# Performance work log

Measured on AMD Instinct MI355X. Metric: run time of the kernel, lower is better.

Reference implementation:

```python
import jax, jax.numpy as jnp
import numpy as np

EPS_LN = 1e-5

def _ln(x, g, b):
    m = x.mean(-1, keepdims=True)
    v = jnp.var(x, axis=-1, keepdims=True)
    return (x - m) * jax.lax.rsqrt(v + EPS_LN) * g + b


def _forward(x, edge_attr, lin0_w, lin0_b, enn_w1, enn_b1, enn_g1, enn_b1n,
             enn_w2, enn_b2, enn_g2, enn_b2n, conv_bias,
             gru_w_ih, gru_w_hh, gru_b_ih, gru_b_hh,
             lstm_w_ih, lstm_w_hh, lstm_b_ih, lstm_b_hh,
             lin1_w, lin1_b, lin1_g, lin1_bn, lin2_w, lin2_b,
             edge_index, target_index, target_class):
    N = x.shape[0]
    D = lin0_w.shape[0]
    src, dst = edge_index[0], edge_index[1]

    out = jax.nn.relu(x @ lin0_w.T + lin0_b)            # [N, D]
    h = out                                             # GRU hidden state

    # edge NN -> per-edge weight matrix [E, D, D] (edge_attr constant across iters)
    e1 = jax.nn.relu(_ln(edge_attr @ enn_w1.T + enn_b1, enn_g1, enn_b1n))
    ew = _ln(e1 @ enn_w2.T + enn_b2, enn_g2, enn_b2n).reshape(-1, D, D)

    counts = jnp.clip(jax.ops.segment_sum(jnp.ones_like(dst, jnp.float32), dst, num_segments=N), 1.0)[:, None]

    for _ in range(3):
        msg = jnp.einsum('ed,edo->eo', out[src], ew)     # per-edge matmul
        agg = jax.ops.segment_sum(msg, dst, num_segments=N) / counts  # scatter-mean
        m = jax.nn.relu(agg + conv_bias)
        # GRU cell (seq len 1)
        gx = m @ gru_w_ih.T + gru_b_ih
        gh = h @ gru_w_hh.T + gru_b_hh
        xr, xz, xn = jnp.split(gx, 3, axis=-1)
        hr, hz, hn = jnp.split(gh, 3, axis=-1)
        r = jax.nn.sigmoid(xr + hr)
        z = jax.nn.sigmoid(xz + hz)
        n = jnp.tanh(xn + r * hn)
        h = (1.0 - z) * n + z * h
        out = h

    # Set2Set with batch_index = arange(N) (each node is its own set), 3 steps
    idx = jnp.arange(N)
    hl = jnp.zeros((N, D), x.dtype)
    cl = jnp.zeros((N, D), x.dtype)
    q_star = jnp.zeros((N, 2 * D), x.dtype)
    for _ in range(3):
        g = q_star @ lstm_w_ih.T + lstm_b_ih + hl @ lstm_w_hh.T + lstm_b_hh
        gi, gf, gg, go = jnp.split(g, 4, axis=-1)
        cl = jax.nn.sigmoid(gf) * cl + jax.nn.sigmoid(gi) * jnp.tanh(gg)
        hl = jax.nn.sigmoid(go) * jnp.tanh(cl)
        q = hl
        e = (out * q[idx]).sum(-1, keepdims=True)
        emax = jax.ops.segment_max(e, idx, num_segments=N)
        a = jnp.exp(e - emax[idx])
        a = a / (jax.ops.segment_sum(a, idx, num_segments=N)[idx] + 1e-16)
        r_pool = jax.ops.segment_sum(a * out, idx, num_segments=N)
        q_star = jnp.concatenate([q, r_pool], axis=-1)

    a0, a1 = target_index[0], target_index[1]
    cat = jnp.concatenate([out[a0], out[a1], q_star[a0], q_star[a1]], axis=-1)  # [P, 6D]
    p = jax.nn.relu(_ln(cat @ lin1_w.T + lin1_b, lin1_g, lin1_bn))
    p = p @ lin2_w.T + lin2_b                           # [P, 8]
    return jnp.take_along_axis(p, target_class[:, None], axis=1)[:, 0]


def setup_inputs() -> dict:
    N, E, P, F, D = 10000, 20000, 15000, 16, 64
    ks = iter(jax.random.split(jax.random.key(0), 40))
    def nrm(shape, s=0.1):
        return jax.random.normal(next(ks), shape, jnp.float32) * s
    return {
        'x': jax.random.normal(next(ks), (N, F), jnp.float32),
        'edge_attr': jax.random.normal(next(ks), (E, 4), jnp.float32),
        'lin0_w': nrm((D, F)), 'lin0_b': jnp.zeros((D,), jnp.float32),
        'enn_w1': nrm((128, 4)), 'enn_b1': jnp.zeros((128,), jnp.float32),
        'enn_g1': jnp.ones((128,), jnp.float32), 'enn_b1n': jnp.zeros((128,), jnp.float32),
        'enn_w2': nrm((D * D, 128), 0.05), 'enn_b2': jnp.zeros((D * D,), jnp.float32),
        'enn_g2': jnp.ones((D * D,), jnp.float32), 'enn_b2n': jnp.zeros((D * D,), jnp.float32),
        'conv_bias': jnp.zeros((D,), jnp.float32),
        'gru_w_ih': nrm((3 * D, D)), 'gru_w_hh': nrm((3 * D, D)),
        'gru_b_ih': jnp.zeros((3 * D,), jnp.float32), 'gru_b_hh': jnp.zeros((3 * D,), jnp.float32),
        'lstm_w_ih': nrm((4 * D, 2 * D)), 'lstm_w_hh': nrm((4 * D, D)),
        'lstm_b_ih': jnp.zeros((4 * D,), jnp.float32), 'lstm_b_hh': jnp.zeros((4 * D,), jnp.float32),
        'lin1_w': nrm((D, 6 * D)), 'lin1_b': jnp.zeros((D,), jnp.float32),
        'lin1_g': jnp.ones((D,), jnp.float32), 'lin1_bn': jnp.zeros((D,), jnp.float32),
        'lin2_w': nrm((8, D)), 'lin2_b': jnp.zeros((8,), jnp.float32),
        'edge_index': jax.random.randint(next(ks), (2, E), 0, N),
        'target_index': jax.random.randint(next(ks), (2, P), 0, N),
        'target_class': jax.random.randint(next(ks), (P,), 0, 8),
    }


def reference(x, edge_attr, lin0_w, lin0_b, enn_w1, enn_b1, enn_g1, enn_b1n,
              enn_w2, enn_b2, enn_g2, enn_b2n, conv_bias,
              gru_w_ih, gru_w_hh, gru_b_ih, gru_b_hh,
              lstm_w_ih, lstm_w_hh, lstm_b_ih, lstm_b_hh,
              lin1_w, lin1_b, lin1_g, lin1_bn, lin2_w, lin2_b,
              edge_index, target_index, target_class):
    return _forward(x, edge_attr, lin0_w, lin0_b, enn_w1, enn_b1, enn_g1, enn_b1n,
                    enn_w2, enn_b2, enn_g2, enn_b2n, conv_bias,
                    gru_w_ih, gru_w_hh, gru_b_ih, gru_b_hh,
                    lstm_w_ih, lstm_w_hh, lstm_b_ih, lstm_b_hh,
                    lin1_w, lin1_b, lin1_g, lin1_bn, lin2_w, lin2_b,
                    edge_index, target_index, target_class)
```

## Files before the change

### kernel.cpp

```cpp
#include <hip/hip_runtime.h>
#include <hip/hip_bf16.h>

#define EPS_LN 1e-5f

typedef __attribute__((ext_vector_type(8))) short bf16x8;
typedef __attribute__((ext_vector_type(4))) float f32x4;

__device__ __forceinline__ float dot4(float4 a, float4 b) {
    return a.x * b.x + a.y * b.y + a.z * b.z + a.w * b.w;
}
__device__ __forceinline__ float sigmoidf_(float x) { return 1.0f / (1.0f + expf(-x)); }

__device__ __forceinline__ float bfu2f(unsigned short u) {
    unsigned v = ((unsigned)u) << 16;
    float f;
    __builtin_memcpy(&f, &v, 4);
    return f;
}
__device__ __forceinline__ unsigned short f2bfu(float f) {
    __hip_bfloat16 h = __float2bfloat16(f);
    unsigned short u;
    __builtin_memcpy(&u, &h, 2);
    return u;
}
__device__ __forceinline__ unsigned pack2bf(float a, float b) {
    return (unsigned)f2bfu(a) | ((unsigned)f2bfu(b) << 16);
}
__device__ __forceinline__ void async_cp16(void* lds, const void* g) {
    __builtin_amdgcn_global_load_lds((const __attribute__((address_space(1))) void*)g,
                                     (__attribute__((address_space(3))) void*)lds, 16, 0, 0);
}

__global__ void init_kernel(const float* __restrict__ x, const float* __restrict__ w,
                            const float* __restrict__ b, float* __restrict__ h,
                            const int* __restrict__ ei, float* __restrict__ counts,
                            int N, int E) {
    int id = blockIdx.x * blockDim.x + threadIdx.x;
    if (id < N * 64) {
        int n = id >> 6, o = id & 63;
        const float* xr = x + n * 16;
        const float* wr = w + o * 16;
        float acc = b[o];
#pragma unroll
        for (int k = 0; k < 16; k++) acc += xr[k] * wr[k];
        h[id] = fmaxf(acc, 0.0f);
    }
    if (id < E) atomicAdd(&counts[ei[E + id]], 1.0f);
}

__global__ __launch_bounds__(128) void edge_nn1_kernel(
    const float* __restrict__ ea, const float* __restrict__ w1, const float* __restrict__ b1,
    const float* __restrict__ g1, const float* __restrict__ b1n,
    unsigned short* __restrict__ e1h, unsigned short* __restrict__ e1l, int E) {
    int e = blockIdx.x, j = threadIdx.x;
    float a0 = ea[e * 4 + 0], a1 = ea[e * 4 + 1], a2 = ea[e * 4 + 2], a3 = ea[e * 4 + 3];
    const float* wr = w1 + j * 4;
    float z = b1[j] + a0 * wr[0] + a1 * wr[1] + a2 * wr[2] + a3 * wr[3];
    float s = z, s2 = z * z;
#pragma unroll
    for (int m = 32; m >= 1; m >>= 1) { s += __shfl_xor(s, m); s2 += __shfl_xor(s2, m); }
    __shared__ float ls[2], ls2[2];
    int wv = j >> 6;
    if ((j & 63) == 0) { ls[wv] = s; ls2[wv] = s2; }
    __syncthreads();
    float S = ls[0] + ls[1], S2 = ls2[0] + ls2[1];
    float mu = S * (1.0f / 128.0f);
    float var = fmaxf(S2 * (1.0f / 128.0f) - mu * mu, 0.0f);
    float inv = rsqrtf(var + EPS_LN);
    float v = fmaxf((z - mu) * inv * g1[j] + b1n[j], 0.0f);
    unsigned short hi = f2bfu(v);
    unsigned short lo = f2bfu(v - bfu2f(hi));
    int jp = j ^ ((e & 7) << 3);
    e1h[e * 128 + jp] = hi;
    e1l[e * 128 + jp] = lo;
}

__global__ __launch_bounds__(128) void mpart_kernel(const float* __restrict__ w2,
                                                    const float* __restrict__ b2,
                                                    const float* __restrict__ g2,
                                                    unsigned short* __restrict__ w2gp,
                                                    float* __restrict__ b2g,
                                                    float* __restrict__ pMT, float* __restrict__ pv,
                                                    float* __restrict__ pcw, float* __restrict__ psb,
                                                    float* __restrict__ pc) {
    __shared__ float wL[16][128];
    __shared__ float b2L[16];
    int t = threadIdx.x, b = blockIdx.x;
#pragma unroll
    for (int i = 0; i < 16; i++) {
        int idx = t + i * 128;
        wL[idx >> 7][idx & 127] = w2[(size_t)(b * 16 + (idx >> 7)) * 128 + (idx & 127)];
    }
    if (t < 16) b2L[t] = b2[b * 16 + t];
    __syncthreads();
#pragma unroll
    for (int o = 0; o < 16; o++) {
        int r = b * 16 + o;
        int x = (r & 63) >> 1;
        int jj = (r >> 6) + ((r & 1) << 6);
        w2gp[(size_t)x * 16384 + jj * 128 + (t ^ ((jj & 7) << 3))] = f2bfu(wL[o][t] * g2[r]);
    }
    if (t < 16) b2g[b * 16 + t] = b2L[t] * g2[b * 16 + t];
    int j = t;
    float wj[16];
#pragma unroll
    for (int o = 0; o < 16; o++) wj[o] = wL[o][j];
    float pvj = 0.f, pcwj = 0.f;
#pragma unroll
    for (int o = 0; o < 16; o++) { pvj += wj[o] * b2L[o]; pcwj += wj[o]; }
    for (int i4 = 0; i4 < 32; i4++) {
        float4 a = {0.f, 0.f, 0.f, 0.f};
#pragma unroll
        for (int o = 0; o < 16; o++) {
            float4 w4 = *(const float4*)&wL[o][i4 * 4];
            a.x += wj[o] * w4.x; a.y += wj[o] * w4.y;
            a.z += wj[o] * w4.z; a.w += wj[o] * w4.w;
        }
        *(float4*)&pMT[((size_t)b * 128 + j) * 128 + i4 * 4] = a;
    }
    pv[b * 128 + j] = pvj;
    pcw[b * 128 + j] = pcwj;
    if (t == 0) {
        float sb = 0.f, cc = 0.f;
#pragma unroll
        for (int o = 0; o < 16; o++) { sb += b2L[o]; cc += b2L[o] * b2L[o]; }
        psb[b] = sb;
        pc[b] = cc;
    }
}

__global__ __launch_bounds__(256) void mreduce_kernel(const float* __restrict__ pMT,
                                                      const float* __restrict__ pv,
                                                      const float* __restrict__ pcw,
                                                      const float* __restrict__ psb,
                                                      const float* __restrict__ pc,
                                                      unsigned short* __restrict__ mb,
                                                      float* __restrict__ varr,
                                                      float* __restrict__ cw,
                                                      float* __restrict__ sbc) {
    int fid = blockIdx.x * 256 + threadIdx.x;
    float s = 0.f;
    int j = fid >> 7, i = fid & 127;
    for (int b = 0; b < 256; b++) s += pMT[((size_t)b * 128 + j) * 128 + i];
    mb[fid] = f2bfu(s);
    if (fid < 128) {
        float sv = 0.f, sc = 0.f;
        for (int b = 0; b < 256; b++) { sv += pv[b * 128 + fid]; sc += pcw[b * 128 + fid]; }
        varr[fid] = sv;
        cw[fid] = sc;
    }
    if (fid == 0) {
        float sb = 0.f, cc = 0.f;
        for (int b = 0; b < 256; b++) { sb += psb[b]; cc += pc[b]; }
        sbc[0] = sb;
        sbc[1] = cc;
    }
}

__global__ __launch_bounds__(256) void stats_kernel(
    const unsigned short* __restrict__ e1h, const unsigned short* __restrict__ e1l,
    const unsigned short* __restrict__ mb, const float* __restrict__ cw,
    const float* __restrict__ varr, const float* __restrict__ sbc,
    float* __restrict__ stats, int E) {
    __shared__ __align__(16) unsigned char smem[65536];
    const int t = threadIdx.x;
    const int eb = blockIdx.x * 64;
#pragma unroll
    for (int r = 0; r < 4; r++) {
        int idx = t + r * 256;
        int row = idx >> 4, kseg = idx & 15;
        int er = eb + row;
        if (er >= E) er = E - 1;
        uint4 vh = *(const uint4*)&e1h[(size_t)er * 128 + kseg * 8];
        uint4 vl = *(const uint4*)&e1l[(size_t)er * 128 + kseg * 8];
        int off = row * 256 + kseg * 16;
        *(uint4*)(smem + off) = vh;
        *(uint4*)(smem + 16384 + off) = vl;
    }
#pragma unroll
    for (int r = 0; r < 8; r++) {
        int idx = t + r * 256;
        int row = idx >> 4, kseg = idx & 15;
        uint4 v = *(const uint4*)&mb[(size_t)row * 128 + kseg * 8];
        *(uint4*)(smem + 32768 + row * 256 + ((kseg * 16) ^ ((row & 7) << 4))) = v;
    }
    __syncthreads();
    const int w = t >> 6, lane = t & 63;
    const int wrow = w * 16;
    const int r16 = lane & 15, kg = lane >> 4;
    f32x4 tacc[8];
#pragma unroll
    for (int nj = 0; nj < 8; nj++) tacc[nj] = (f32x4){0.f, 0.f, 0.f, 0.f};
#pragma unroll
    for (int ks = 0; ks < 4; ks++) {
        int arow = wrow + r16;
        int koff = ks * 64 + kg * 16;
        bf16x8 ah = *(const bf16x8*)(smem + arow * 256 + (koff ^ ((arow & 7) << 4)));
        bf16x8 al = *(const bf16x8*)(smem + 16384 + arow * 256 + (koff ^ ((arow & 7) << 4)));
#pragma unroll
        for (int nj = 0; nj < 8; nj++) {
            int brow = nj * 16 + r16;
            bf16x8 bf = *(const bf16x8*)(smem + 32768 + brow * 256 + (koff ^ ((brow & 7) << 4)));
            tacc[nj] = __builtin_amdgcn_mfma_f32_16x16x32_bf16(ah, bf, tacc[nj], 0, 0, 0);
            tacc[nj] = __builtin_amdgcn_mfma_f32_16x16x32_bf16(al, bf, tacc[nj], 0, 0, 0);
        }
    }
    __syncthreads();
#pragma unroll
    for (int nj = 0; nj < 8; nj++)
#pragma unroll
        for (int r = 0; r < 4; r++) {
            int row = wrow + kg * 4 + r, col = nj * 16 + r16;
            *(float*)(smem + 32768 + row * 512 + col * 4) = tacc[nj][r];
        }
    __syncthreads();
    int el = t >> 2, q = t & 3;
    float s2p = 0.f, sp = 0.f, svp = 0.f;
    for (int kk = 0; kk < 32; kk++) {
        int k = q * 32 + kk;
        int boff = el * 256 + ((2 * k) ^ ((el & 7) << 4));
        float e1v = bfu2f(*(const unsigned short*)(smem + boff)) +
                    bfu2f(*(const unsigned short*)(smem + 16384 + boff));
        float tv = *(const float*)(smem + 32768 + el * 512 + k * 4);
        s2p += tv * e1v;
        sp += e1v * cw[k];
        svp += e1v * varr[k];
    }
    s2p += __shfl_xor(s2p, 1); s2p += __shfl_xor(s2p, 2);
    sp += __shfl_xor(sp, 1);   sp += __shfl_xor(sp, 2);
    svp += __shfl_xor(svp, 1); svp += __shfl_xor(svp, 2);
    if (q == 0) {
        int e = eb + el;
        if (e < E) {
            float S = sp + sbc[0];
            float S2 = s2p + 2.f * svp + sbc[1];
            float mu = S * (1.0f / 4096.0f);
            float var = fmaxf(S2 * (1.0f / 4096.0f) - mu * mu, 0.0f);
            float inv = rsqrtf(var + EPS_LN);
            stats[e * 2 + 0] = inv;
            stats[e * 2 + 1] = mu * inv;
        }
    }
}

__global__ __launch_bounds__(256) void zgemm_final(
    const unsigned short* __restrict__ e1h,
    const unsigned short* __restrict__ w2gp, const float* __restrict__ b2g,
    const float* __restrict__ g2, const float* __restrict__ b2n,
    const float* __restrict__ stats, unsigned short* __restrict__ zT, int E) {
    __shared__ __align__(16) unsigned char smem[49152];
    __shared__ float cBg[128], cGg[128], cBn[128];
    __shared__ float sInv[64], sMiv[64];
    const int t = threadIdx.x;
    const int w = t >> 6, lane = t & 63;
    const int eb = blockIdx.y * 64;
    const int cb = blockIdx.x * 128;
    const int o0 = blockIdx.x * 2;
    {
        const char* srcA = (const char*)e1h + (size_t)eb * 256 + w * 1024 + lane * 16;
        char* dstA = (char*)smem + w * 1024 + lane * 16;
#pragma unroll
        for (int i = 0; i < 4; i++) async_cp16(dstA + i * 4096, srcA + i * 4096);
        const char* srcB = (const char*)w2gp + (size_t)blockIdx.x * 32768 + w * 1024 + lane * 16;
        char* dstB = (char*)smem + 16384 + w * 1024 + lane * 16;
#pragma unroll
        for (int i = 0; i < 8; i++) async_cp16(dstB + i * 4096, srcB + i * 4096);
    }
    if (t < 128) {
        int sj = ((t & 63) << 6) + o0 + (t >> 6);
        cBg[t] = b2g[sj];
        cGg[t] = g2[sj];
        cBn[t] = b2n[sj];
    } else if (t < 192) {
        int tt = t - 128;
        int eg = eb + tt;
        if (eg >= E) eg = E - 1;
        sInv[tt] = stats[eg * 2 + 0];
        sMiv[tt] = stats[eg * 2 + 1];
    }
    __syncthreads();
    const int wrow = (w >> 1) * 32, wcol = (w & 1) * 64;
    const int r16 = lane & 15, kg = lane >> 4;

    f32x4 acc[2][4];
#pragma unroll
    for (int mi = 0; mi < 2; mi++)
#pragma unroll
        for (int nj = 0; nj < 4; nj++) acc[mi][nj] = (f32x4){0.f, 0.f, 0.f, 0.f};
#pragma unroll
    for (int ks = 0; ks < 4; ks++) {
        int koff = ks * 64 + kg * 16;
        bf16x8 af[2];
#pragma unroll
        for (int mi = 0; mi < 2; mi++) {
            int row = wrow + mi * 16 + r16;
            af[mi] = *(const bf16x8*)(smem + row * 256 + (koff ^ ((row & 7) << 4)));
        }
        bf16x8 bf[4];
#pragma unroll
        for (int nj = 0; nj < 4; nj++) {
            int row = wcol + nj * 16 + r16;
            bf[nj] = *(const bf16x8*)(smem + 16384 + row * 256 + (koff ^ ((row & 7) << 4)));
        }
#pragma unroll
        for (int mi = 0; mi < 2; mi++)
#pragma unroll
            for (int nj = 0; nj < 4; nj++)
                acc[mi][nj] = __builtin_amdgcn_mfma_f32_16x16x32_bf16(
                    bf[nj], af[mi], acc[mi][nj], 0, 0, 0);
    }
#pragma unroll
    for (int mi = 0; mi < 2; mi++) {
        int e_local = wrow + mi * 16 + r16;
        int e = eb + e_local;
        float inv = sInv[e_local], miv = sMiv[e_local];
        bool ok = (e < E);
#pragma unroll
        for (int nj = 0; nj < 4; nj++) {
            int j0 = wcol + nj * 16 + kg * 4;
            float4 bg4 = *(const float4*)&cBg[j0];
            float4 gg4 = *(const float4*)&cGg[j0];
            float4 bn4 = *(const float4*)&cBn[j0];
            ushort4 sv;
            sv.x = f2bfu(inv * (acc[mi][nj][0] + bg4.x) - miv * gg4.x + bn4.x);
            sv.y = f2bfu(inv * (acc[mi][nj][1] + bg4.y) - miv * gg4.y + bn4.y);
            sv.z = f2bfu(inv * (acc[mi][nj][2] + bg4.z) - miv * gg4.z + bn4.z);
            sv.w = f2bfu(inv * (acc[mi][nj][3] + bg4.w) - miv * gg4.w + bn4.w);
            if (ok) *(ushort4*)&zT[(size_t)e * 4096 + cb + j0] = sv;
        }
    }
}

__global__ __launch_bounds__(256) void msg_kernel(const unsigned short* __restrict__ zT,
                                                  const float* __restrict__ h,
                                                  const int* __restrict__ ei,
                                                  float* __restrict__ agg, int E) {
    int t = threadIdx.x;
    int w = t >> 6, lane = t & 63;
    int e = blockIdx.x * 4 + w;
    __shared__ float hL[4][64];
    __shared__ float oL[4][64];
    int src = ei[e];
    int dstn = ei[E + e];
    hL[w][lane] = h[(size_t)src * 64 + lane];
    __syncthreads();
    const uint4* zp = (const uint4*)(zT + (size_t)e * 4096);
    const int d0 = (lane & 7) * 8;
    const float* hp = &hL[w][d0];
    float h0 = hp[0], h1v = hp[1], h2 = hp[2], h3 = hp[3];
    float h4 = hp[4], h5 = hp[5], h6 = hp[6], h7 = hp[7];
    float accq[8];
#pragma unroll
    for (int q = 0; q < 8; q++) {
        uint4 v = zp[q * 64 + lane];
        float a;
        a  = __uint_as_float(v.x << 16) * h0 + __uint_as_float(v.x & 0xffff0000u) * h1v;
        a += __uint_as_float(v.y << 16) * h2 + __uint_as_float(v.y & 0xffff0000u) * h3;
        a += __uint_as_float(v.z << 16) * h4 + __uint_as_float(v.z & 0xffff0000u) * h5;
        a += __uint_as_float(v.w << 16) * h6 + __uint_as_float(v.w & 0xffff0000u) * h7;
        accq[q] = a;
    }
#pragma unroll
    for (int q = 0; q < 8; q++) {
        accq[q] += __shfl_xor(accq[q], 1);
        accq[q] += __shfl_xor(accq[q], 2);
        accq[q] += __shfl_xor(accq[q], 4);
    }
    if ((lane & 7) == 0) {
#pragma unroll
        for (int q = 0; q < 8; q++) oL[w][q * 8 + (lane >> 3)] = accq[q];
    }
    __syncthreads();
    atomicAdd(&agg[(size_t)dstn * 64 + lane], oL[w][lane]);
}

__global__ __launch_bounds__(192) void gru_kernel(
    const float* __restrict__ agg, const float* __restrict__ counts, const float* __restrict__ cbias,
    const float* __restrict__ wih, const float* __restrict__ whh,
    const float* __restrict__ bih, const float* __restrict__ bhh, float* __restrict__ h, int N) {
    int t = threadIdx.x;
    int nb = blockIdx.x * 8;
    __shared__ __align__(16) float mL[8][64], hL[8][64], gxL[8][192], ghL[8][192];
    for (int idx = t; idx < 512; idx += 192) {
        int n = idx >> 6, k = idx & 63;
        int node = nb + n;
        float cnt = fmaxf(counts[node], 1.0f);
        mL[n][k] = fmaxf(agg[node * 64 + k] / cnt + cbias[k], 0.0f);
        hL[n][k] = h[node * 64 + k];
    }
    __syncthreads();
    {
        int j = t;
        float ax[8], ah[8];
#pragma unroll
        for (int n = 0; n < 8; n++) { ax[n] = 0.f; ah[n] = 0.f; }
        const float4* wi = (const float4*)(wih + j * 64);
        const float4* wh = (const float4*)(whh + j * 64);
#pragma unroll 4
        for (int k4 = 0; k4 < 16; k4++) {
            float4 wiv = wi[k4], whv = wh[k4];
#pragma unroll
            for (int n = 0; n < 8; n++) {
                ax[n] += dot4(wiv, *(const float4*)&mL[n][k4 * 4]);
                ah[n] += dot4(whv, *(const float4*)&hL[n][k4 * 4]);
            }
        }
        float bi = bih[j], bh = bhh[j];
#pragma unroll
        for (int n = 0; n < 8; n++) { gxL[n][j] = ax[n] + bi; ghL[n][j] = ah[n] + bh; }
    }
    __syncthreads();
    for (int idx = t; idx < 512; idx += 192) {
        int n = idx >> 6, k = idx & 63;
        int node = nb + n;
        float r = sigmoidf_(gxL[n][k] + ghL[n][k]);
        float zz = sigmoidf_(gxL[n][64 + k] + ghL[n][64 + k]);
        float nn = tanhf(gxL[n][128 + k] + r * ghL[n][128 + k]);
        h[node * 64 + k] = (1.0f - zz) * nn + zz * hL[n][k];
    }
}

__global__ __launch_bounds__(256) void coutprep_kernel(
    const float* __restrict__ h, const float* __restrict__ wih, const float* __restrict__ whh,
    const float* __restrict__ bih, const float* __restrict__ bhh,
    float* __restrict__ cout, float* __restrict__ wc,
    float* __restrict__ hl, float* __restrict__ cl, int N) {
    int t = threadIdx.x, nb = blockIdx.x * 8;
    __shared__ __align__(16) float oL[8][64];
    for (int idx = t; idx < 512; idx += 256) {
        int n = idx >> 6, k = idx & 63;
        oL[n][k] = h[(nb + n) * 64 + k];
    }
    __syncthreads();
    {
        float acc[8];
#pragma unroll
        for (int n = 0; n < 8; n++) acc[n] = 0.f;
        const float* wr = wih + t * 128 + 64;
#pragma unroll 4
        for (int k4 = 0; k4 < 16; k4++) {
            float4 w4 = *(const float4*)&wr[k4 * 4];
#pragma unroll
            for (int n = 0; n < 8; n++) acc[n] += dot4(w4, *(const float4*)&oL[n][k4 * 4]);
        }
#pragma unroll
        for (int n = 0; n < 8; n++) cout[(size_t)(nb + n) * 256 + t] = acc[n];
    }
    if (blockIdx.x < 64) {
        int id = blockIdx.x * 256 + t;
        int j = id >> 6, k = id & 63;
        wc[id] = wih[j * 128 + k] + whh[id];
    }
    if (t < 64) {
        float gi = bih[t] + bhh[t];
        float gg = bih[128 + t] + bhh[128 + t];
        float go = bih[192 + t] + bhh[192 + t];
        float c0 = sigmoidf_(gi) * tanhf(gg);
        float h0 = sigmoidf_(go) * tanhf(c0);
#pragma unroll
        for (int n = 0; n < 8; n++) {
            cl[(nb + n) * 64 + t] = c0;
            hl[(nb + n) * 64 + t] = h0;
        }
    }
}

__global__ __launch_bounds__(256) void lstm_step_kernel(const float* __restrict__ wc,
                                                        const float* __restrict__ bih,
                                                        const float* __restrict__ bhh,
                                                        const float* __restrict__ cout,
                                                        float* __restrict__ hl,
                                                        float* __restrict__ cl, int N) {
    int t = threadIdx.x, nb = blockIdx.x * 8;
    __shared__ __align__(16) float hlL[8][64];
    __shared__ float gL[8][256];
    for (int idx = t; idx < 512; idx += 256) {
        int n = idx >> 6, k = idx & 63;
        hlL[n][k] = hl[(nb + n) * 64 + k];
    }
    __syncthreads();
    {
        float acc[8];
#pragma unroll
        for (int n = 0; n < 8; n++) acc[n] = 0.f;
        const float4* w4p = (const float4*)(wc + t * 64);
#pragma unroll 4
        for (int k4 = 0; k4 < 16; k4++) {
            float4 w4 = w4p[k4];
#pragma unroll
            for (int n = 0; n < 8; n++) acc[n] += dot4(w4, *(const float4*)&hlL[n][k4 * 4]);
        }
        float bs = bih[t] + bhh[t];
#pragma unroll
        for (int n = 0; n < 8; n++) gL[n][t] = acc[n] + cout[(size_t)(nb + n) * 256 + t] + bs;
    }
    __syncthreads();
    for (int idx = t; idx < 512; idx += 256) {
        int n = idx >> 6, k = idx & 63;
        int node = nb + n;
        float gi = gL[n][k], gf = gL[n][64 + k], gg = gL[n][128 + k], go = gL[n][192 + k];
        float c = sigmoidf_(gf) * cl[node * 64 + k] + sigmoidf_(gi) * tanhf(gg);
        cl[node * 64 + k] = c;
        hl[node * 64 + k] = sigmoidf_(go) * tanhf(c);
    }
}

__global__ __launch_bounds__(256) void head_kernel(
    const float* __restrict__ h, const float* __restrict__ hl, const int* __restrict__ ti,
    const int* __restrict__ tc, const float* __restrict__ w1, const float* __restrict__ b1,
    const float* __restrict__ g1, const float* __restrict__ bn1, const float* __restrict__ w2,
    const float* __restrict__ b2, float* __restrict__ out, int P) {
    __shared__ uint2 w1q[6144];
    __shared__ float catL[4][384];
    int t = threadIdx.x;
    const float4* w1f4 = (const float4*)w1;
#pragma unroll
    for (int i = 0; i < 24; i++) {
        int f = t + i * 256;
        float4 v = w1f4[f];
        int j = f / 96, k4 = f - j * 96;
        w1q[k4 * 64 + j] = make_uint2(pack2bf(v.x, v.y), pack2bf(v.z, v.w));
    }
    int j = t & 63, pl = t >> 6;
    float b1j = b1[j], g1j = g1[j], bnj = bn1[j];
    __syncthreads();

    for (int pb = blockIdx.x * 4; pb < P; pb += gridDim.x * 4) {
#pragma unroll
        for (int i = 0; i < 6; i++) {
            int idx = t + i * 256;
            int p = idx / 384, kk = idx - p * 384;
            int pair = pb + p;
            if (pair >= P) pair = P - 1;
            int a0 = ti[pair], a1 = ti[P + pair];
            int s = kk >> 6, k = kk & 63;
            float v;
            if (s == 0 || s == 3) v = h[a0 * 64 + k];
            else if (s == 1 || s == 5) v = h[a1 * 64 + k];
            else if (s == 2) v = hl[a0 * 64 + k];
            else v = hl[a1 * 64 + k];
            catL[p][kk] = v;
        }
        __syncthreads();
        int pair = pb + pl;
        float acc = b1j;
#pragma unroll 8
        for (int k4 = 0; k4 < 96; k4++) {
            uint2 wv = w1q[k4 * 64 + j];
            float4 c = *(const float4*)&catL[pl][k4 * 4];
            acc += __uint_as_float(wv.x << 16) * c.x + __uint_as_float(wv.x & 0xffff0000u) * c.y;
            acc += __uint_as_float(wv.y << 16) * c.z + __uint_as_float(wv.y & 0xffff0000u) * c.w;
        }
        float s1 = acc, s2v = acc * acc;
#pragma unroll
        for (int m = 32; m >= 1; m >>= 1) { s1 += __shfl_xor(s1, m); s2v += __shfl_xor(s2v, m); }
        float mu = s1 * (1.0f / 64.0f);
        float var = fmaxf(s2v * (1.0f / 64.0f) - mu * mu, 0.0f);
        float p1 = fmaxf((acc - mu) * rsqrtf(var + EPS_LN) * g1j + bnj, 0.0f);
        int cls = tc[pair < P ? pair : P - 1];
        float part = p1 * w2[cls * 64 + j];
#pragma unroll
        for (int m = 32; m >= 1; m >>= 1) part += __shfl_xor(part, m);
        if (j == 0 && pair < P) out[pair] = part + b2[cls];
        __syncthreads();
    }
}

extern "C" void kernel_launch(void* const* d_in, const int* in_sizes, int n_in,
                              void* d_out, int out_size, void* d_ws, size_t ws_size,
                              hipStream_t stream) {
    const float* x = (const float*)d_in[0];
    const float* edge_attr = (const float*)d_in[1];
    const float* lin0_w = (const float*)d_in[2];
    const float* lin0_b = (const float*)d_in[3];
    const float* enn_w1 = (const float*)d_in[4];
    const float* enn_b1 = (const float*)d_in[5];
    const float* enn_g1 = (const float*)d_in[6];
    const float* enn_b1n = (const float*)d_in[7];
    const float* enn_w2 = (const float*)d_in[8];
    const float* enn_b2 = (const float*)d_in[9];
    const float* enn_g2 = (const float*)d_in[10];
    const float* enn_b2n = (const float*)d_in[11];
    const float* conv_bias = (const float*)d_in[12];
    const float* gru_w_ih = (const float*)d_in[13];
    const float* gru_w_hh = (const float*)d_in[14];
    const float* gru_b_ih = (const float*)d_in[15];
    const float* gru_b_hh = (const float*)d_in[16];
    const float* lstm_w_ih = (const float*)d_in[17];
    const float* lstm_w_hh = (const float*)d_in[18];
    const float* lstm_b_ih = (const float*)d_in[19];
    const float* lstm_b_hh = (const float*)d_in[20];
    const float* lin1_w = (const float*)d_in[21];
    const float* lin1_b = (const float*)d_in[22];
    const float* lin1_g = (const float*)d_in[23];
    const float* lin1_bn = (const float*)d_in[24];
    const float* lin2_w = (const float*)d_in[25];
    const float* lin2_b = (const float*)d_in[26];
    const int* edge_index = (const int*)d_in[27];
    const int* target_index = (const int*)d_in[28];
    const int* target_class = (const int*)d_in[29];

    const int N = in_sizes[0] / 16;
    const int E = in_sizes[27] / 2;
    const int P = in_sizes[29];

    size_t off = 0;
    auto carve = [&](size_t bytes) {
        void* p = (char*)d_ws + off;
        off += (bytes + 255) & ~(size_t)255;
        return p;
    };
    unsigned short* zbuf = (unsigned short*)carve((size_t)E * 4096 * 2);
    unsigned short* e1h = (unsigned short*)carve((size_t)E * 128 * 2);
    unsigned short* e1l = (unsigned short*)carve((size_t)E * 128 * 2);
    unsigned short* w2gp = (unsigned short*)carve((size_t)4096 * 128 * 2);
    float* b2g = (float*)carve((size_t)4096 * 4);
    float* hbuf = (float*)carve((size_t)N * 64 * 4);
    float* counts = (float*)carve((size_t)N * 4 + (size_t)3 * N * 64 * 4);
    float* agg0 = counts + N;
    float* agg1 = agg0 + (size_t)N * 64;
    float* agg2 = agg1 + (size_t)N * 64;
    float* hl = (float*)carve((size_t)N * 64 * 4);
    float* cl = (float*)carve((size_t)N * 64 * 4);
    float* cout_b = (float*)carve((size_t)N * 256 * 4);
    float* wc = (float*)carve((size_t)256 * 64 * 4);
    float* stats = (float*)carve((size_t)E * 2 * 4);
    unsigned short* mb = (unsigned short*)carve((size_t)128 * 128 * 2);
    float* varr = (float*)carve((size_t)128 * 4);
    float* cw = (float*)carve((size_t)128 * 4);
    float* sbc = (float*)carve((size_t)2 * 4);
    float* pv = (float*)carve((size_t)256 * 128 * 4);
    float* pcw = (float*)carve((size_t)256 * 128 * 4);
    float* psb = (float*)carve((size_t)256 * 4);
    float* pc = (float*)carve((size_t)256 * 4);
    float* pMT = (float*)carve((size_t)256 * 128 * 128 * 4);
    (void)ws_size;

    hipMemsetAsync(counts, 0, (size_t)N * 4 + (size_t)3 * N * 64 * 4, stream);
    init_kernel<<<(N * 64 + 255) / 256, 256, 0, stream>>>(x, lin0_w, lin0_b, hbuf, edge_index,
                                                          counts, N, E);
    edge_nn1_kernel<<<E, 128, 0, stream>>>(edge_attr, enn_w1, enn_b1, enn_g1, enn_b1n, e1h, e1l, E);
    mpart_kernel<<<256, 128, 0, stream>>>(enn_w2, enn_b2, enn_g2, w2gp, b2g, pMT, pv, pcw, psb, pc);
    mreduce_kernel<<<64, 256, 0, stream>>>(pMT, pv, pcw, psb, pc, mb, varr, cw, sbc);
    stats_kernel<<<(E + 63) / 64, 256, 0, stream>>>(e1h, e1l, mb, cw, varr, sbc, stats, E);
    {
        dim3 g(32, (E + 63) / 64);
        zgemm_final<<<g, 256, 0, stream>>>(e1h, w2gp, b2g, enn_g2, enn_b2n, stats, zbuf, E);
    }

    float* aggs[3] = {agg0, agg1, agg2};
    for (int it = 0; it < 3; it++) {
        msg_kernel<<<E / 4, 256, 0, stream>>>(zbuf, hbuf, edge_index, aggs[it], E);
        gru_kernel<<<N / 8, 192, 0, stream>>>(aggs[it], counts, conv_bias, gru_w_ih, gru_w_hh,
                                              gru_b_ih, gru_b_hh, hbuf, N);
    }

    coutprep_kernel<<<N / 8, 256, 0, stream>>>(hbuf, lstm_w_ih, lstm_w_hh, lstm_b_ih, lstm_b_hh,
                                               cout_b, wc, hl, cl, N);
    lstm_step_kernel<<<N / 8, 256, 0, stream>>>(wc, lstm_b_ih, lstm_b_hh, cout_b, hl, cl, N);
    lstm_step_kernel<<<N / 8, 256, 0, stream>>>(wc, lstm_b_ih, lstm_b_hh, cout_b, hl, cl, N);

    head_kernel<<<512, 256, 0, stream>>>(hbuf, hl, target_index, target_class, lin1_w, lin1_b,
                                         lin1_g, lin1_bn, lin2_w, lin2_b, (float*)d_out, P);
}
```

Baseline: 380.7 us.

## Fuse first message-passing iteration into edge-weight GEMM epilogue

The edge-weight GEMM epilogue now dots each computed weight row with the source node's hidden state and atomically accumulates the per-edge message into the first aggregation buffer. This removes one full msg_kernel pass, which would have re-read the entire bf16 per-edge weight tensor from memory. In exchange the GEMM epilogue carries extra loads of node features, cross-lane shuffles and many global float atomics. It also uses unrounded fp32 weights for the first iteration rather than the stored bf16 values.

```diff
diff --git a/kernel.cpp b/kernel.cpp
--- a/kernel.cpp
+++ b/kernel.cpp
@@ -247,10 +247,13 @@
     const unsigned short* __restrict__ e1h,
     const unsigned short* __restrict__ w2gp, const float* __restrict__ b2g,
     const float* __restrict__ g2, const float* __restrict__ b2n,
-    const float* __restrict__ stats, unsigned short* __restrict__ zT, int E) {
+    const float* __restrict__ stats, const float* __restrict__ h1,
+    const int* __restrict__ ei, float* __restrict__ agg0,
+    unsigned short* __restrict__ zT, int E) {
     __shared__ __align__(16) unsigned char smem[49152];
     __shared__ float cBg[128], cGg[128], cBn[128];
     __shared__ float sInv[64], sMiv[64];
+    __shared__ int sSrc[64], sDst[64];
     const int t = threadIdx.x;
     const int w = t >> 6, lane = t & 63;
     const int eb = blockIdx.y * 64;
@@ -277,10 +280,28 @@
         if (eg >= E) eg = E - 1;
         sInv[tt] = stats[eg * 2 + 0];
         sMiv[tt] = stats[eg * 2 + 1];
+    } else {
+        int tt = t - 192;
+        int eg = eb + tt;
+        if (eg >= E) eg = E - 1;
+        sSrc[tt] = ei[eg];
+        sDst[tt] = ei[E + eg];
     }
     __syncthreads();
     const int wrow = (w >> 1) * 32, wcol = (w & 1) * 64;
+    const int og = o0 + (w & 1);
     const int r16 = lane & 15, kg = lane >> 4;
+
+    float4 h4[2][4];
+#pragma unroll
+    for (int mi = 0; mi < 2; mi++) {
+        int src = sSrc[wrow + mi * 16 + r16];
+#pragma unroll
+        for (int nj = 0; nj < 4; nj++) {
+            int d0 = nj * 16 + kg * 4;
+            h4[mi][nj] = *(const float4*)&h1[(size_t)src * 64 + d0];
+        }
+    }
 
     f32x4 acc[2][4];
 #pragma unroll
@@ -315,19 +336,26 @@
         int e = eb + e_local;
         float inv = sInv[e_local], miv = sMiv[e_local];
         bool ok = (e < E);
+        float pm = 0.f;
 #pragma unroll
         for (int nj = 0; nj < 4; nj++) {
             int j0 = wcol + nj * 16 + kg * 4;
             float4 bg4 = *(const float4*)&cBg[j0];
             float4 gg4 = *(const float4*)&cGg[j0];
             float4 bn4 = *(const float4*)&cBn[j0];
+            float v0 = inv * (acc[mi][nj][0] + bg4.x) - miv * gg4.x + bn4.x;
+            float v1 = inv * (acc[mi][nj][1] + bg4.y) - miv * gg4.y + bn4.y;
+            float v2 = inv * (acc[mi][nj][2] + bg4.z) - miv * gg4.z + bn4.z;
+            float v3 = inv * (acc[mi][nj][3] + bg4.w) - miv * gg4.w + bn4.w;
+            float4 hv = h4[mi][nj];
+            pm += v0 * hv.x + v1 * hv.y + v2 * hv.z + v3 * hv.w;
             ushort4 sv;
-            sv.x = f2bfu(inv * (acc[mi][nj][0] + bg4.x) - miv * gg4.x + bn4.x);
-            sv.y = f2bfu(inv * (acc[mi][nj][1] + bg4.y) - miv * gg4.y + bn4.y);
-            sv.z = f2bfu(inv * (acc[mi][nj][2] + bg4.z) - miv * gg4.z + bn4.z);
-            sv.w = f2bfu(inv * (acc[mi][nj][3] + bg4.w) - miv * gg4.w + bn4.w);
+            sv.x = f2bfu(v0); sv.y = f2bfu(v1); sv.z = f2bfu(v2); sv.w = f2bfu(v3);
             if (ok) *(ushort4*)&zT[(size_t)e * 4096 + cb + j0] = sv;
         }
+        pm += __shfl_xor(pm, 16);
+        pm += __shfl_xor(pm, 32);
+        if (ok && kg == 0) atomicAdd(&agg0[(size_t)sDst[e_local] * 64 + og], pm);
     }
 }
 
@@ -645,11 +673,14 @@
     stats_kernel<<<(E + 63) / 64, 256, 0, stream>>>(e1h, e1l, mb, cw, varr, sbc, stats, E);
     {
         dim3 g(32, (E + 63) / 64);
-        zgemm_final<<<g, 256, 0, stream>>>(e1h, w2gp, b2g, enn_g2, enn_b2n, stats, zbuf, E);
-    }
-
-    float* aggs[3] = {agg0, agg1, agg2};
-    for (int it = 0; it < 3; it++) {
+        zgemm_final<<<g, 256, 0, stream>>>(e1h, w2gp, b2g, enn_g2, enn_b2n, stats, hbuf,
+                                           edge_index, agg0, zbuf, E);
+    }
+
+    gru_kernel<<<N / 8, 192, 0, stream>>>(agg0, counts, conv_bias, gru_w_ih, gru_w_hh,
+                                          gru_b_ih, gru_b_hh, hbuf, N);
+    float* aggs[2] = {agg1, agg2};
+    for (int it = 0; it < 2; it++) {
         msg_kernel<<<E / 4, 256, 0, stream>>>(zbuf, hbuf, edge_index, aggs[it], E);
         gru_kernel<<<N / 8, 192, 0, stream>>>(aggs[it], counts, conv_bias, gru_w_ih, gru_w_hh,
                                               gru_b_ih, gru_b_hh, hbuf, N);
```

After: 409.6 us. +7.6%, slower.

## Reuse B weight fragments across multiple edge tiles per zgemm block

Applied to the files above, without the earlier changes.

Each zgemm_final block now walks ZTILES=4 consecutive 64-edge tiles. It loads the w2 weight slice into shared memory once and keeps its MFMA fragments in registers for all four tiles, instead of reloading the slice for every tile. The next A tile is prefetched asynchronously while the current tile's epilogue runs. This cuts redundant weight traffic and block launch overhead, but leaves a quarter as many blocks, adds per-tile barriers and raises register pressure, which may lower occupancy.

```diff
diff --git a/kernel.cpp b/kernel.cpp
--- a/kernel.cpp
+++ b/kernel.cpp
@@ -2,6 +2,7 @@
 #include <hip/hip_bf16.h>
 
 #define EPS_LN 1e-5f
+#define ZTILES 4
 
 typedef __attribute__((ext_vector_type(8))) short bf16x8;
 typedef __attribute__((ext_vector_type(4))) float f32x4;
@@ -250,84 +251,100 @@
     const float* __restrict__ stats, unsigned short* __restrict__ zT, int E) {
     __shared__ __align__(16) unsigned char smem[49152];
     __shared__ float cBg[128], cGg[128], cBn[128];
-    __shared__ float sInv[64], sMiv[64];
     const int t = threadIdx.x;
     const int w = t >> 6, lane = t & 63;
-    const int eb = blockIdx.y * 64;
     const int cb = blockIdx.x * 128;
     const int o0 = blockIdx.x * 2;
+    const int soff = w * 1024 + lane * 16;
+    int eb = blockIdx.y * (ZTILES * 64);
     {
-        const char* srcA = (const char*)e1h + (size_t)eb * 256 + w * 1024 + lane * 16;
-        char* dstA = (char*)smem + w * 1024 + lane * 16;
+        const char* srcB = (const char*)w2gp + (size_t)blockIdx.x * 32768 + soff;
+        char* dstB = (char*)smem + 16384 + soff;
+#pragma unroll
+        for (int i = 0; i < 8; i++) async_cp16(dstB + i * 4096, srcB + i * 4096);
+        const char* srcA = (const char*)e1h + (size_t)eb * 256 + soff;
+        char* dstA = (char*)smem + soff;
 #pragma unroll
         for (int i = 0; i < 4; i++) async_cp16(dstA + i * 4096, srcA + i * 4096);
-        const char* srcB = (const char*)w2gp + (size_t)blockIdx.x * 32768 + w * 1024 + lane * 16;
-        char* dstB = (char*)smem + 16384 + w * 1024 + lane * 16;
-#pragma unroll
-        for (int i = 0; i < 8; i++) async_cp16(dstB + i * 4096, srcB + i * 4096);
     }
     if (t < 128) {
         int sj = ((t & 63) << 6) + o0 + (t >> 6);
         cBg[t] = b2g[sj];
         cGg[t] = g2[sj];
         cBn[t] = b2n[sj];
-    } else if (t < 192) {
-        int tt = t - 128;
-        int eg = eb + tt;
-        if (eg >= E) eg = E - 1;
-        sInv[tt] = stats[eg * 2 + 0];
-        sMiv[tt] = stats[eg * 2 + 1];
     }
     __syncthreads();
     const int wrow = (w >> 1) * 32, wcol = (w & 1) * 64;
     const int r16 = lane & 15, kg = lane >> 4;
-
-    f32x4 acc[2][4];
-#pragma unroll
-    for (int mi = 0; mi < 2; mi++)
-#pragma unroll
-        for (int nj = 0; nj < 4; nj++) acc[mi][nj] = (f32x4){0.f, 0.f, 0.f, 0.f};
-#pragma unroll
-    for (int ks = 0; ks < 4; ks++) {
-        int koff = ks * 64 + kg * 16;
-        bf16x8 af[2];
+    bf16x8 bfrag[4][4];
+#pragma unroll
+    for (int nj = 0; nj < 4; nj++)
+#pragma unroll
+        for (int ks = 0; ks < 4; ks++) {
+            int row = wcol + nj * 16 + r16;
+            int koff = ks * 64 + kg * 16;
+            bfrag[nj][ks] = *(const bf16x8*)(smem + 16384 + row * 256 + (koff ^ ((row & 7) << 4)));
+        }
+#pragma unroll 1
+    for (int ti = 0; ti < ZTILES; ti++, eb += 64) {
+        if (eb >= E) break;
+        float sInvR[2], sMivR[2];
 #pragma unroll
         for (int mi = 0; mi < 2; mi++) {
-            int row = wrow + mi * 16 + r16;
-            af[mi] = *(const bf16x8*)(smem + row * 256 + (koff ^ ((row & 7) << 4)));
-        }
-        bf16x8 bf[4];
-#pragma unroll
-        for (int nj = 0; nj < 4; nj++) {
-            int row = wcol + nj * 16 + r16;
-            bf[nj] = *(const bf16x8*)(smem + 16384 + row * 256 + (koff ^ ((row & 7) << 4)));
-        }
+            int eg = eb + wrow + mi * 16 + r16;
+            if (eg >= E) eg = E - 1;
+            sInvR[mi] = stats[eg * 2 + 0];
+            sMivR[mi] = stats[eg * 2 + 1];
+        }
+        f32x4 acc[2][4];
 #pragma unroll
         for (int mi = 0; mi < 2; mi++)
 #pragma unroll
-            for (int nj = 0; nj < 4; nj++)
-                acc[mi][nj] = __builtin_amdgcn_mfma_f32_16x16x32_bf16(
-                    bf[nj], af[mi], acc[mi][nj], 0, 0, 0);
-    }
-#pragma unroll
-    for (int mi = 0; mi < 2; mi++) {
-        int e_local = wrow + mi * 16 + r16;
-        int e = eb + e_local;
-        float inv = sInv[e_local], miv = sMiv[e_local];
-        bool ok = (e < E);
-#pragma unroll
-        for (int nj = 0; nj < 4; nj++) {
-            int j0 = wcol + nj * 16 + kg * 4;
-            float4 bg4 = *(const float4*)&cBg[j0];
-            float4 gg4 = *(const float4*)&cGg[j0];
-            float4 bn4 = *(const float4*)&cBn[j0];
-            ushort4 sv;
-            sv.x = f2bfu(inv * (acc[mi][nj][0] + bg4.x) - miv * gg4.x + bn4.x);
-            sv.y = f2bfu(inv * (acc[mi][nj][1] + bg4.y) - miv * gg4.y + bn4.y);
-            sv.z = f2bfu(inv * (acc[mi][nj][2] + bg4.z) - miv * gg4.z + bn4.z);
-            sv.w = f2bfu(inv * (acc[mi][nj][3] + bg4.w) - miv * gg4.w + bn4.w);
-            if (ok) *(ushort4*)&zT[(size_t)e * 4096 + cb + j0] = sv;
-        }
+            for (int nj = 0; nj < 4; nj++) acc[mi][nj] = (f32x4){0.f, 0.f, 0.f, 0.f};
+#pragma unroll
+        for (int ks = 0; ks < 4; ks++) {
+            int koff = ks * 64 + kg * 16;
+            bf16x8 af[2];
+#pragma unroll
+            for (int mi = 0; mi < 2; mi++) {
+                int row = wrow + mi * 16 + r16;
+                af[mi] = *(const bf16x8*)(smem + row * 256 + (koff ^ ((row & 7) << 4)));
+            }
+#pragma unroll
+            for (int mi = 0; mi < 2; mi++)
+#pragma unroll
+                for (int nj = 0; nj < 4; nj++)
+                    acc[mi][nj] = __builtin_amdgcn_mfma_f32_16x16x32_bf16(
+                        bfrag[nj][ks], af[mi], acc[mi][nj], 0, 0, 0);
+        }
+        __syncthreads();
+        if (ti + 1 < ZTILES && eb + 64 < E) {
+            const char* srcA = (const char*)e1h + (size_t)(eb + 64) * 256 + soff;
+            char* dstA = (char*)smem + soff;
+#pragma unroll
+            for (int i = 0; i < 4; i++) async_cp16(dstA + i * 4096, srcA + i * 4096);
+        }
+#pragma unroll
+        for (int mi = 0; mi < 2; mi++) {
+            int e_local = wrow + mi * 16 + r16;
+            int e = eb + e_local;
+            float inv = sInvR[mi], miv = sMivR[mi];
+            bool ok = (e < E);
+#pragma unroll
+            for (int nj = 0; nj < 4; nj++) {
+                int j0 = wcol + nj * 16 + kg * 4;
+                float4 bg4 = *(const float4*)&cBg[j0];
+                float4 gg4 = *(const float4*)&cGg[j0];
+                float4 bn4 = *(const float4*)&cBn[j0];
+                ushort4 sv;
+                sv.x = f2bfu(inv * (acc[mi][nj][0] + bg4.x) - miv * gg4.x + bn4.x);
+                sv.y = f2bfu(inv * (acc[mi][nj][1] + bg4.y) - miv * gg4.y + bn4.y);
+                sv.z = f2bfu(inv * (acc[mi][nj][2] + bg4.z) - miv * gg4.z + bn4.z);
+                sv.w = f2bfu(inv * (acc[mi][nj][3] + bg4.w) - miv * gg4.w + bn4.w);
+                if (ok) *(ushort4*)&zT[(size_t)e * 4096 + cb + j0] = sv;
+            }
+        }
+        __syncthreads();
     }
 }
 
@@ -644,7 +661,8 @@
     mreduce_kernel<<<64, 256, 0, stream>>>(pMT, pv, pcw, psb, pc, mb, varr, cw, sbc);
     stats_kernel<<<(E + 63) / 64, 256, 0, stream>>>(e1h, e1l, mb, cw, varr, sbc, stats, E);
     {
-        dim3 g(32, (E + 63) / 64);
+        int NT = (E + 63) / 64;
+        dim3 g(32, (NT + ZTILES - 1) / ZTILES);
         zgemm_final<<<g, 256, 0, stream>>>(e1h, w2gp, b2g, enn_g2, enn_b2n, stats, zbuf, E);
     }
 
```

After: 373.5 us. No clear change (-1.9%).
